# Kernel optimization log

Measured on AMD Instinct MI355X. Metric: run time of the kernel, lower is better.

## Reference

```python
import jax, jax.numpy as jnp
import numpy as np

REL_SIZE = 65
TAG_SIZE = 4


def _rope(y):
    # Interleaved rotary position embedding, matching the torch module:
    # cos_pos = cos(theta) repeat_interleave(2), sin_pos = sin(theta) repeat_interleave(2)
    # y2 = (-y1, y0, -y3, y2, ...)
    B, S, H = y.shape
    half = H // 2
    pos = jnp.arange(S, dtype=jnp.float32)[:, None]                      # (S,1)
    inv_freq = jnp.power(10000.0, -2.0 * jnp.arange(half, dtype=jnp.float32) / H)
    theta = pos * inv_freq                                               # (S, half)
    cos = jnp.repeat(jnp.cos(theta), 2, axis=-1)                          # (S, H)
    sin = jnp.repeat(jnp.sin(theta), 2, axis=-1)                          # (S, H)
    yr = y.reshape(B, S, half, 2)
    y2 = jnp.stack([-yr[..., 1], yr[..., 0]], axis=-1).reshape(B, S, H)
    return y * cos + y2 * sin


def setup_inputs() -> dict:
    key = jax.random.key(0)
    k1, k2, k3 = jax.random.split(key, 3)
    B, S, H = 1, 160, 768
    y = jax.random.normal(k1, (B, S, H), dtype=jnp.float32)
    event_idx = jax.random.randint(k2, (B, 16), 0, S)
    W1 = jax.random.normal(k3, (H, 2 * H), dtype=jnp.float32) * 0.02
    b1 = jnp.zeros((H,), dtype=jnp.float32)
    W2 = jax.random.normal(jax.random.fold_in(key, 7), (REL_SIZE * TAG_SIZE, H), dtype=jnp.float32) * 0.02
    b2 = jnp.zeros((REL_SIZE * TAG_SIZE,), dtype=jnp.float32)
    return {"y": y, "event_idx": event_idx, "W1": W1, "b1": b1, "W2": W2, "b2": b2}


def reference(y, event_idx, W1, b1, W2, b2):
    # Eval path (training=False): event_idx unused, dropout = identity, sigmoid applied.
    B, S, H = y.shape
    yrot = _rope(y)
    # Linear(cat(a, b)) is separable: split W1 into the halves acting on a and b.
    Wa, Wb = W1[:, :H], W1[:, H:]
    left = jnp.einsum('bsh,oh->bso', yrot, Wa)                  # contribution of token i (row)
    right = jnp.einsum('bsh,oh->bso', yrot, Wb) + b1            # contribution of token j (col)
    h = jax.nn.relu(left[:, :, None, :] + right[:, None, :, :])  # (B, S, S, H)
    out = jnp.einsum('bijh,oh->bijo', h, W2) + b2               # (B, S, S, 260)
    out = out.reshape(B, S, S, REL_SIZE, TAG_SIZE).transpose(0, 3, 1, 2, 4)  # (B, 65, S, S, 4)
    return jax.nn.sigmoid(out)
```

## Files before the change

### kernel.cpp

```cpp
#include <hip/hip_runtime.h>
#include <hip/hip_bf16.h>
#include <cstdint>

#define SDIM 160
#define HDIM 768
#define HALF 384
#define ODIM 260
#define OPAD 272
#define WS_SMALL 1155088
#define WS_BIG   3514384

typedef __attribute__((ext_vector_type(8))) short short8;
typedef __attribute__((ext_vector_type(4))) float floatx4;
typedef _Float16 half8 __attribute__((ext_vector_type(8)));

static __device__ __forceinline__ float bf2f(unsigned short u) {
    union { unsigned int i; float f; } v; v.i = ((unsigned int)u) << 16; return v.f;
}
static __device__ __forceinline__ unsigned short f2bf(float x) {
    __hip_bfloat16 h = __float2bfloat16(x);
    return *reinterpret_cast<unsigned short*>(&h);
}
static __device__ __forceinline__ unsigned short f2h(float x) {
    _Float16 h = (_Float16)x;
    return *reinterpret_cast<unsigned short*>(&h);
}
static __device__ __forceinline__ float q(float x) { return bf2f(f2bf(x)); }

__global__ __launch_bounds__(256) void prep_kernel(
    const float* __restrict__ y, const float* __restrict__ W1,
    const float* __restrict__ W2,
    unsigned short* __restrict__ yb, unsigned short* __restrict__ W2b,
    unsigned short* __restrict__ W1b, int do_w1b) {
    int bid = blockIdx.x;
    int t = threadIdx.x;
    if (bid < SDIM) {
        int s = bid;
        for (int p = t; p < HALF; p += 256) {
            float invf = __expf(-(2.0f * (float)p / (float)HDIM) * 9.210340371976184f);
            float th = (float)s * invf;
            float c = cosf(th), sn = sinf(th);
            float y0 = y[s * HDIM + 2 * p], y1 = y[s * HDIM + 2 * p + 1];
            yb[s * HDIM + 2 * p]     = f2bf(y0 * c - y1 * sn);
            yb[s * HDIM + 2 * p + 1] = f2bf(y1 * c + y0 * sn);
        }
    } else if (bid < SDIM + 102) {
        int idx = (bid - SDIM) * 256 + t;
        if (idx < 96 * OPAD) {
            int kg = idx / OPAD, row = idx - kg * OPAD;
            unsigned short o8[8];
            if (row < ODIM) {
                float4 a = *reinterpret_cast<const float4*>(W2 + row * HDIM + kg * 8);
                float4 b = *reinterpret_cast<const float4*>(W2 + row * HDIM + kg * 8 + 4);
                o8[0] = f2h(a.x); o8[1] = f2h(a.y); o8[2] = f2h(a.z); o8[3] = f2h(a.w);
                o8[4] = f2h(b.x); o8[5] = f2h(b.y); o8[6] = f2h(b.z); o8[7] = f2h(b.w);
            } else {
                #pragma unroll
                for (int e = 0; e < 8; ++e) o8[e] = 0;
            }
            *reinterpret_cast<uint4*>(W2b + ((size_t)kg * OPAD + row) * 8) =
                *reinterpret_cast<uint4*>(o8);
        }
    } else if (do_w1b) {
        int idx = (bid - SDIM - 102) * 256 + t;
        int kg = idx / 1536, row = idx - kg * 1536;
        const float* src = (row < 768) ? (W1 + row * 1536 + kg * 8)
                                       : (W1 + (row - 768) * 1536 + 768 + kg * 8);
        float4 a = *reinterpret_cast<const float4*>(src);
        float4 b = *reinterpret_cast<const float4*>(src + 4);
        unsigned short o8[8];
        o8[0] = f2bf(a.x); o8[1] = f2bf(a.y); o8[2] = f2bf(a.z); o8[3] = f2bf(a.w);
        o8[4] = f2bf(b.x); o8[5] = f2bf(b.y); o8[6] = f2bf(b.z); o8[7] = f2bf(b.w);
        *reinterpret_cast<uint4*>(W1b + ((size_t)kg * 1536 + row) * 8) =
            *reinterpret_cast<uint4*>(o8);
    }
}

__global__ __launch_bounds__(64, 2) void lr3_kernel(
    const unsigned short* __restrict__ yb, const unsigned short* __restrict__ W1b,
    const float* __restrict__ b1,
    unsigned short* __restrict__ Lb, unsigned short* __restrict__ Rt) {
    int l = threadIdx.x & 63;
    int l16 = l & 15, qd = l >> 4;
    int mt = blockIdx.x;
    int sq = blockIdx.y;
    int s0 = sq * 16 + l16;

    floatx4 acc = (floatx4){0.0f, 0.0f, 0.0f, 0.0f};

    const unsigned short* yrow0 = yb + s0 * HDIM;

    for (int ks = 0; ks < 24; ++ks) {
        int k = ks * 32 + qd * 8;
        int kg = ks * 4 + qd;
        union { uint4 u; short8 s; } bu0, au;
        bu0.u = *reinterpret_cast<const uint4*>(yrow0 + k);
        au.u = *reinterpret_cast<const uint4*>(
            W1b + ((size_t)kg * 1536 + mt * 16 + l16) * 8);
        acc = __builtin_amdgcn_mfma_f32_16x16x32_bf16(
            au.s, bu0.s, acc, 0, 0, 0);
    }

    int o2 = mt * 16 + qd * 4;
    int s_out = sq * 16 + l16;
    unsigned short out4[4];
    if (o2 < 768) {
        #pragma unroll
        for (int r = 0; r < 4; ++r) out4[r] = f2h(acc[r]);
        *reinterpret_cast<uint2*>(Lb + s_out * HDIM + o2) =
            *reinterpret_cast<uint2*>(out4);
    } else {
        int ob = o2 - 768;
        #pragma unroll
        for (int r = 0; r < 4; ++r)
            out4[r] = f2h(acc[r] + b1[ob + r]);
        *reinterpret_cast<uint2*>(
            Rt + ((size_t)(ob >> 3) * SDIM + s_out) * 8 + (ob & 7)) =
            *reinterpret_cast<uint2*>(out4);
    }
}

__global__ __launch_bounds__(256) void lr_fallback_kernel(
    const unsigned short* __restrict__ yb, const float* __restrict__ W1,
    const float* __restrict__ b1,
    unsigned short* __restrict__ Lb, unsigned short* __restrict__ Rt) {
    int idx = blockIdx.x * 256 + threadIdx.x;
    int s = idx / 1536;
    int o2 = idx - s * 1536;
    const unsigned short* yrow = yb + s * HDIM;
    if (o2 < 768) {
        const float* wp = W1 + o2 * 1536;
        float a0 = 0.0f;
        for (int k = 0; k < HDIM; ++k) a0 += q(wp[k]) * bf2f(yrow[k]);
        Lb[s * HDIM + o2] = f2h(a0);
    } else {
        int ob = o2 - 768;
        const float* wp = W1 + ob * 1536 + 768;
        float a0 = 0.0f;
        for (int k = 0; k < HDIM; ++k) a0 += q(wp[k]) * bf2f(yrow[k]);
        Rt[((size_t)(ob >> 3) * SDIM + s) * 8 + (ob & 7)] = f2h(a0 + b1[ob]);
    }
}

__global__ __launch_bounds__(64, 4) void main_kernel(
    const unsigned short* __restrict__ Lb, const unsigned short* __restrict__ Rt,
    const unsigned short* __restrict__ W2b,
    const float* __restrict__ b2, float* __restrict__ out) {
    int l = threadIdx.x & 63;
    int l16 = l & 15, qd = l >> 4;
    int w = blockIdx.z;
    int jh = w & 1;
    int mq = w >> 1;
    int mt0 = mq * 4;
    int nmt = (mq == 3) ? 5 : 4;
    int i0 = blockIdx.x * 2;
    int j = blockIdx.y * 32 + jh * 16 + l16;

    floatx4 acc[2][5];
    #pragma unroll
    for (int c = 0; c < 2; ++c)
        #pragma unroll
        for (int mtl = 0; mtl < 5; ++mtl)
            acc[c][mtl] = (floatx4){0.0f, 0.0f, 0.0f, 0.0f};

    const unsigned short* Lrow0 = Lb + i0 * HDIM;
    const unsigned short* Lrow1 = Lb + (i0 + 1) * HDIM;
    const unsigned short* wbase = W2b + (size_t)l16 * 8;

    #pragma unroll 2
    for (int kc = 0; kc < 12; ++kc) {
        #pragma unroll
        for (int ks = 0; ks < 2; ++ks) {
            int k = kc * 64 + ks * 32 + qd * 8;
            int kg = kc * 8 + ks * 4 + qd;
            half8 bfrag[2];
            union { uint4 u; half8 h; } ru;
            ru.u = *reinterpret_cast<const uint4*>(
                Rt + ((size_t)kg * SDIM + j) * 8);
            #pragma unroll
            for (int c = 0; c < 2; ++c) {
                const unsigned short* Lr = c ? Lrow1 : Lrow0;
                union { uint4 u; half8 h; } lu;
                lu.u = *reinterpret_cast<const uint4*>(Lr + k);
                half8 hv = lu.h + ru.h;
                #pragma unroll
                for (int e = 0; e < 8; ++e)
                    hv[e] = hv[e] > (_Float16)0.0f ? hv[e] : (_Float16)0.0f;
                bfrag[c] = hv;
            }
            const unsigned short* wkg = wbase + (size_t)kg * OPAD * 8;
            #pragma unroll
            for (int mtl = 0; mtl < 5; ++mtl) {
                if (mtl < nmt) {
                    union { uint4 u; half8 h; } au;
                    au.u = *reinterpret_cast<const uint4*>(
                        wkg + (size_t)(mt0 + mtl) * 16 * 8);
                    acc[0][mtl] = __builtin_amdgcn_mfma_f32_16x16x32_f16(
                        au.h, bfrag[0], acc[0][mtl], 0, 0, 0);
                    acc[1][mtl] = __builtin_amdgcn_mfma_f32_16x16x32_f16(
                        au.h, bfrag[1], acc[1][mtl], 0, 0, 0);
                }
            }
        }
    }

    #pragma unroll
    for (int c = 0; c < 2; ++c) {
        int i = i0 + c;
        #pragma unroll
        for (int mtl = 0; mtl < 5; ++mtl) {
            if (mtl < nmt) {
                int ob = (mt0 + mtl) * 16 + qd * 4;
                if (ob < ODIM) {
                    float4 bv = *reinterpret_cast<const float4*>(b2 + ob);
                    int rel = ob >> 2;
                    float4 v;
                    v.x = 1.0f / (1.0f + __expf(-(acc[c][mtl][0] + bv.x)));
                    v.y = 1.0f / (1.0f + __expf(-(acc[c][mtl][1] + bv.y)));
                    v.z = 1.0f / (1.0f + __expf(-(acc[c][mtl][2] + bv.z)));
                    v.w = 1.0f / (1.0f + __expf(-(acc[c][mtl][3] + bv.w)));
                    *reinterpret_cast<float4*>(
                        out + (((rel * SDIM) + i) * SDIM + j) * 4) = v;
                }
            }
        }
    }
}

__global__ void ws_too_small_kernel(float* out) { out[0] = 999.0f; }

extern "C" void kernel_launch(void* const* d_in, const int* in_sizes, int n_in,
                              void* d_out, int out_size, void* d_ws, size_t ws_size,
                              hipStream_t stream) {
    const float* y  = (const float*)d_in[0];
    const float* W1 = (const float*)d_in[2];
    const float* b1 = (const float*)d_in[3];
    const float* W2 = (const float*)d_in[4];
    const float* b2 = (const float*)d_in[5];
    float* out = (float*)d_out;

    if (ws_size < (size_t)WS_SMALL) {
        ws_too_small_kernel<<<dim3(1), dim3(1), 0, stream>>>(out);
        return;
    }

    unsigned short* yb  = (unsigned short*)((char*)d_ws + 16);
    unsigned short* Lb  = yb + SDIM * HDIM;
    unsigned short* Rt  = Lb + SDIM * HDIM;
    unsigned short* W2b = Rt + SDIM * HDIM;
    unsigned short* W1b = W2b + 96 * OPAD * 8;

    if (ws_size >= (size_t)WS_BIG) {
        prep_kernel<<<dim3(SDIM + 102 + 576), dim3(256), 0, stream>>>(
            y, W1, W2, yb, W2b, W1b, 1);
        lr3_kernel<<<dim3(96, 10), dim3(64), 0, stream>>>(yb, W1b, b1, Lb, Rt);
        main_kernel<<<dim3(80, 5, 8), dim3(64), 0, stream>>>(Lb, Rt, W2b, b2, out);
    } else {
        prep_kernel<<<dim3(SDIM + 102), dim3(256), 0, stream>>>(
            y, W1, W2, yb, W2b, W1b, 0);
        lr_fallback_kernel<<<dim3(960), dim3(256), 0, stream>>>(yb, W1, b1, Lb, Rt);
        main_kernel<<<dim3(80, 5, 8), dim3(64), 0, stream>>>(Lb, Rt, W2b, b2, out);
    }
}
```

Baseline: 122.7 us.

## Fuse RoPE/W1 prep into left-right GEMM and double-buffer main kernel loads

The separate prep and left/right projection kernels are merged into one launch. It converts W2 to fp16 and, for each tile, applies RoPE to y and converts W1 to bf16 on the fly before the MFMA. That removes the yb and W1b staging buffers and one kernel launch, at the cost of recomputing sin/cos and W1 conversions redundantly across blocks. The main kernel now prefetches the next k-step's W2, R and L fragments into a second register buffer while the current step's MFMAs run. Its occupancy hint drops from 4 to 3 waves, and every wave now issues all 5 M-tiles regardless of group, so groups that own only 4 tiles do extra discarded MFMA work.

```diff
diff --git a/kernel.cpp b/kernel.cpp
--- a/kernel.cpp
+++ b/kernel.cpp
@@ -7,8 +7,7 @@
 #define HALF 384
 #define ODIM 260
 #define OPAD 272
-#define WS_SMALL 1155088
-#define WS_BIG   3514384
+#define WS_NEED 1155088
 
 typedef __attribute__((ext_vector_type(8))) short short8;
 typedef __attribute__((ext_vector_type(4))) float floatx4;
@@ -25,89 +24,80 @@
     _Float16 h = (_Float16)x;
     return *reinterpret_cast<unsigned short*>(&h);
 }
-static __device__ __forceinline__ float q(float x) { return bf2f(f2bf(x)); }
-
-__global__ __launch_bounds__(256) void prep_kernel(
+
+__global__ __launch_bounds__(64) void fused_a_kernel(
     const float* __restrict__ y, const float* __restrict__ W1,
-    const float* __restrict__ W2,
-    unsigned short* __restrict__ yb, unsigned short* __restrict__ W2b,
-    unsigned short* __restrict__ W1b, int do_w1b) {
+    const float* __restrict__ b1, const float* __restrict__ W2,
+    unsigned short* __restrict__ W2b,
+    unsigned short* __restrict__ Lb, unsigned short* __restrict__ Rt) {
     int bid = blockIdx.x;
     int t = threadIdx.x;
-    if (bid < SDIM) {
-        int s = bid;
-        for (int p = t; p < HALF; p += 256) {
-            float invf = __expf(-(2.0f * (float)p / (float)HDIM) * 9.210340371976184f);
-            float th = (float)s * invf;
-            float c = cosf(th), sn = sinf(th);
-            float y0 = y[s * HDIM + 2 * p], y1 = y[s * HDIM + 2 * p + 1];
-            yb[s * HDIM + 2 * p]     = f2bf(y0 * c - y1 * sn);
-            yb[s * HDIM + 2 * p + 1] = f2bf(y1 * c + y0 * sn);
-        }
-    } else if (bid < SDIM + 102) {
-        int idx = (bid - SDIM) * 256 + t;
-        if (idx < 96 * OPAD) {
-            int kg = idx / OPAD, row = idx - kg * OPAD;
-            unsigned short o8[8];
-            if (row < ODIM) {
-                float4 a = *reinterpret_cast<const float4*>(W2 + row * HDIM + kg * 8);
-                float4 b = *reinterpret_cast<const float4*>(W2 + row * HDIM + kg * 8 + 4);
-                o8[0] = f2h(a.x); o8[1] = f2h(a.y); o8[2] = f2h(a.z); o8[3] = f2h(a.w);
-                o8[4] = f2h(b.x); o8[5] = f2h(b.y); o8[6] = f2h(b.z); o8[7] = f2h(b.w);
-            } else {
-                #pragma unroll
-                for (int e = 0; e < 8; ++e) o8[e] = 0;
-            }
-            *reinterpret_cast<uint4*>(W2b + ((size_t)kg * OPAD + row) * 8) =
-                *reinterpret_cast<uint4*>(o8);
-        }
-    } else if (do_w1b) {
-        int idx = (bid - SDIM - 102) * 256 + t;
-        int kg = idx / 1536, row = idx - kg * 1536;
-        const float* src = (row < 768) ? (W1 + row * 1536 + kg * 8)
-                                       : (W1 + (row - 768) * 1536 + 768 + kg * 8);
-        float4 a = *reinterpret_cast<const float4*>(src);
-        float4 b = *reinterpret_cast<const float4*>(src + 4);
+
+    if (bid < 408) {
+        int idx = bid * 64 + t;
+        int kg = idx / OPAD, row = idx - kg * OPAD;
         unsigned short o8[8];
-        o8[0] = f2bf(a.x); o8[1] = f2bf(a.y); o8[2] = f2bf(a.z); o8[3] = f2bf(a.w);
-        o8[4] = f2bf(b.x); o8[5] = f2bf(b.y); o8[6] = f2bf(b.z); o8[7] = f2bf(b.w);
-        *reinterpret_cast<uint4*>(W1b + ((size_t)kg * 1536 + row) * 8) =
+        if (row < ODIM) {
+            float4 a = *reinterpret_cast<const float4*>(W2 + row * HDIM + kg * 8);
+            float4 b = *reinterpret_cast<const float4*>(W2 + row * HDIM + kg * 8 + 4);
+            o8[0] = f2h(a.x); o8[1] = f2h(a.y); o8[2] = f2h(a.z); o8[3] = f2h(a.w);
+            o8[4] = f2h(b.x); o8[5] = f2h(b.y); o8[6] = f2h(b.z); o8[7] = f2h(b.w);
+        } else {
+            #pragma unroll
+            for (int e = 0; e < 8; ++e) o8[e] = 0;
+        }
+        *reinterpret_cast<uint4*>(W2b + ((size_t)kg * OPAD + row) * 8) =
             *reinterpret_cast<uint4*>(o8);
-    }
-}
-
-__global__ __launch_bounds__(64, 2) void lr3_kernel(
-    const unsigned short* __restrict__ yb, const unsigned short* __restrict__ W1b,
-    const float* __restrict__ b1,
-    unsigned short* __restrict__ Lb, unsigned short* __restrict__ Rt) {
-    int l = threadIdx.x & 63;
-    int l16 = l & 15, qd = l >> 4;
-    int mt = blockIdx.x;
-    int sq = blockIdx.y;
+        return;
+    }
+
+    int bid2 = bid - 408;
+    int mt = bid2 % 96;
+    int sq = bid2 / 96;
+    int l16 = t & 15, qd = t >> 4;
     int s0 = sq * 16 + l16;
+    int row = mt * 16 + l16;
+    const float* wrow = (row < 768) ? (W1 + (size_t)row * 1536)
+                                    : (W1 + (size_t)(row - 768) * 1536 + 768);
+    const float* yrow = y + (size_t)s0 * HDIM;
+    float sf = (float)s0;
 
     floatx4 acc = (floatx4){0.0f, 0.0f, 0.0f, 0.0f};
-
-    const unsigned short* yrow0 = yb + s0 * HDIM;
 
     for (int ks = 0; ks < 24; ++ks) {
         int k = ks * 32 + qd * 8;
         int kg = ks * 4 + qd;
-        union { uint4 u; short8 s; } bu0, au;
-        bu0.u = *reinterpret_cast<const uint4*>(yrow0 + k);
-        au.u = *reinterpret_cast<const uint4*>(
-            W1b + ((size_t)kg * 1536 + mt * 16 + l16) * 8);
-        acc = __builtin_amdgcn_mfma_f32_16x16x32_bf16(
-            au.s, bu0.s, acc, 0, 0, 0);
+        float4 ya = *reinterpret_cast<const float4*>(yrow + k);
+        float4 yb4 = *reinterpret_cast<const float4*>(yrow + k + 4);
+        float yv[8] = {ya.x, ya.y, ya.z, ya.w, yb4.x, yb4.y, yb4.z, yb4.w};
+        unsigned short b8[8];
+        #pragma unroll
+        for (int e = 0; e < 4; ++e) {
+            int p = (k >> 1) + e;
+            float invf = __expf(-(2.0f * (float)p / (float)HDIM) * 9.210340371976184f);
+            float th = sf * invf;
+            float c = cosf(th), sn = sinf(th);
+            float y0 = yv[2 * e], y1 = yv[2 * e + 1];
+            b8[2 * e]     = f2bf(y0 * c - y1 * sn);
+            b8[2 * e + 1] = f2bf(y1 * c + y0 * sn);
+        }
+        float4 wa = *reinterpret_cast<const float4*>(wrow + kg * 8);
+        float4 wb = *reinterpret_cast<const float4*>(wrow + kg * 8 + 4);
+        unsigned short w8[8];
+        w8[0] = f2bf(wa.x); w8[1] = f2bf(wa.y); w8[2] = f2bf(wa.z); w8[3] = f2bf(wa.w);
+        w8[4] = f2bf(wb.x); w8[5] = f2bf(wb.y); w8[6] = f2bf(wb.z); w8[7] = f2bf(wb.w);
+        union { uint4 u; short8 s; } au, bu;
+        au.u = *reinterpret_cast<uint4*>(w8);
+        bu.u = *reinterpret_cast<uint4*>(b8);
+        acc = __builtin_amdgcn_mfma_f32_16x16x32_bf16(au.s, bu.s, acc, 0, 0, 0);
     }
 
     int o2 = mt * 16 + qd * 4;
-    int s_out = sq * 16 + l16;
     unsigned short out4[4];
     if (o2 < 768) {
         #pragma unroll
         for (int r = 0; r < 4; ++r) out4[r] = f2h(acc[r]);
-        *reinterpret_cast<uint2*>(Lb + s_out * HDIM + o2) =
+        *reinterpret_cast<uint2*>(Lb + s0 * HDIM + o2) =
             *reinterpret_cast<uint2*>(out4);
     } else {
         int ob = o2 - 768;
@@ -115,34 +105,12 @@
         for (int r = 0; r < 4; ++r)
             out4[r] = f2h(acc[r] + b1[ob + r]);
         *reinterpret_cast<uint2*>(
-            Rt + ((size_t)(ob >> 3) * SDIM + s_out) * 8 + (ob & 7)) =
+            Rt + ((size_t)(ob >> 3) * SDIM + s0) * 8 + (ob & 7)) =
             *reinterpret_cast<uint2*>(out4);
     }
 }
 
-__global__ __launch_bounds__(256) void lr_fallback_kernel(
-    const unsigned short* __restrict__ yb, const float* __restrict__ W1,
-    const float* __restrict__ b1,
-    unsigned short* __restrict__ Lb, unsigned short* __restrict__ Rt) {
-    int idx = blockIdx.x * 256 + threadIdx.x;
-    int s = idx / 1536;
-    int o2 = idx - s * 1536;
-    const unsigned short* yrow = yb + s * HDIM;
-    if (o2 < 768) {
-        const float* wp = W1 + o2 * 1536;
-        float a0 = 0.0f;
-        for (int k = 0; k < HDIM; ++k) a0 += q(wp[k]) * bf2f(yrow[k]);
-        Lb[s * HDIM + o2] = f2h(a0);
-    } else {
-        int ob = o2 - 768;
-        const float* wp = W1 + ob * 1536 + 768;
-        float a0 = 0.0f;
-        for (int k = 0; k < HDIM; ++k) a0 += q(wp[k]) * bf2f(yrow[k]);
-        Rt[((size_t)(ob >> 3) * SDIM + s) * 8 + (ob & 7)] = f2h(a0 + b1[ob]);
-    }
-}
-
-__global__ __launch_bounds__(64, 4) void main_kernel(
+__global__ __launch_bounds__(64, 3) void main_kernel(
     const unsigned short* __restrict__ Lb, const unsigned short* __restrict__ Rt,
     const unsigned short* __restrict__ W2b,
     const float* __restrict__ b2, float* __restrict__ out) {
@@ -167,40 +135,43 @@
     const unsigned short* Lrow1 = Lb + (i0 + 1) * HDIM;
     const unsigned short* wbase = W2b + (size_t)l16 * 8;
 
+    union U { uint4 u; half8 h; };
+    U au[2][5], ru[2], lu[2][2];
+
+    auto ISSUE = [&](int t, int b) {
+        int kg = t * 4 + qd;
+        const unsigned short* wkg = wbase + (size_t)kg * (OPAD * 8);
+        #pragma unroll
+        for (int m = 0; m < 5; ++m)
+            au[b][m].u = *reinterpret_cast<const uint4*>(
+                wkg + (size_t)(mt0 + m) * 128);
+        ru[b].u = *reinterpret_cast<const uint4*>(
+            Rt + ((size_t)kg * SDIM + j) * 8);
+        int k = t * 32 + qd * 8;
+        lu[b][0].u = *reinterpret_cast<const uint4*>(Lrow0 + k);
+        lu[b][1].u = *reinterpret_cast<const uint4*>(Lrow1 + k);
+    };
+
+    ISSUE(0, 0);
     #pragma unroll 2
-    for (int kc = 0; kc < 12; ++kc) {
-        #pragma unroll
-        for (int ks = 0; ks < 2; ++ks) {
-            int k = kc * 64 + ks * 32 + qd * 8;
-            int kg = kc * 8 + ks * 4 + qd;
-            half8 bfrag[2];
-            union { uint4 u; half8 h; } ru;
-            ru.u = *reinterpret_cast<const uint4*>(
-                Rt + ((size_t)kg * SDIM + j) * 8);
+    for (int t = 0; t < 24; ++t) {
+        int b = t & 1;
+        if (t < 23) ISSUE(t + 1, b ^ 1);
+        half8 bfrag[2];
+        #pragma unroll
+        for (int c = 0; c < 2; ++c) {
+            half8 hv = lu[b][c].h + ru[b].h;
             #pragma unroll
-            for (int c = 0; c < 2; ++c) {
-                const unsigned short* Lr = c ? Lrow1 : Lrow0;
-                union { uint4 u; half8 h; } lu;
-                lu.u = *reinterpret_cast<const uint4*>(Lr + k);
-                half8 hv = lu.h + ru.h;
-                #pragma unroll
-                for (int e = 0; e < 8; ++e)
-                    hv[e] = hv[e] > (_Float16)0.0f ? hv[e] : (_Float16)0.0f;
-                bfrag[c] = hv;
-            }
-            const unsigned short* wkg = wbase + (size_t)kg * OPAD * 8;
-            #pragma unroll
-            for (int mtl = 0; mtl < 5; ++mtl) {
-                if (mtl < nmt) {
-                    union { uint4 u; half8 h; } au;
-                    au.u = *reinterpret_cast<const uint4*>(
-                        wkg + (size_t)(mt0 + mtl) * 16 * 8);
-                    acc[0][mtl] = __builtin_amdgcn_mfma_f32_16x16x32_f16(
-                        au.h, bfrag[0], acc[0][mtl], 0, 0, 0);
-                    acc[1][mtl] = __builtin_amdgcn_mfma_f32_16x16x32_f16(
-                        au.h, bfrag[1], acc[1][mtl], 0, 0, 0);
-                }
-            }
+            for (int e = 0; e < 8; ++e)
+                hv[e] = hv[e] > (_Float16)0.0f ? hv[e] : (_Float16)0.0f;
+            bfrag[c] = hv;
+        }
+        #pragma unroll
+        for (int m = 0; m < 5; ++m) {
+            acc[0][m] = __builtin_amdgcn_mfma_f32_16x16x32_f16(
+                au[b][m].h, bfrag[0], acc[0][m], 0, 0, 0);
+            acc[1][m] = __builtin_amdgcn_mfma_f32_16x16x32_f16(
+                au[b][m].h, bfrag[1], acc[1][m], 0, 0, 0);
         }
     }
 
@@ -239,7 +210,7 @@
     const float* b2 = (const float*)d_in[5];
     float* out = (float*)d_out;
 
-    if (ws_size < (size_t)WS_SMALL) {
+    if (ws_size < (size_t)WS_NEED) {
         ws_too_small_kernel<<<dim3(1), dim3(1), 0, stream>>>(out);
         return;
     }
@@ -248,17 +219,8 @@
     unsigned short* Lb  = yb + SDIM * HDIM;
     unsigned short* Rt  = Lb + SDIM * HDIM;
     unsigned short* W2b = Rt + SDIM * HDIM;
-    unsigned short* W1b = W2b + 96 * OPAD * 8;
-
-    if (ws_size >= (size_t)WS_BIG) {
-        prep_kernel<<<dim3(SDIM + 102 + 576), dim3(256), 0, stream>>>(
-            y, W1, W2, yb, W2b, W1b, 1);
-        lr3_kernel<<<dim3(96, 10), dim3(64), 0, stream>>>(yb, W1b, b1, Lb, Rt);
-        main_kernel<<<dim3(80, 5, 8), dim3(64), 0, stream>>>(Lb, Rt, W2b, b2, out);
-    } else {
-        prep_kernel<<<dim3(SDIM + 102), dim3(256), 0, stream>>>(
-            y, W1, W2, yb, W2b, W1b, 0);
-        lr_fallback_kernel<<<dim3(960), dim3(256), 0, stream>>>(yb, W1, b1, Lb, Rt);
-        main_kernel<<<dim3(80, 5, 8), dim3(64), 0, stream>>>(Lb, Rt, W2b, b2, out);
-    }
-}
+
+    fused_a_kernel<<<dim3(408 + 960), dim3(64), 0, stream>>>(
+        y, W1, b1, W2, W2b, Lb, Rt);
+    main_kernel<<<dim3(80, 5, 8), dim3(64), 0, stream>>>(Lb, Rt, W2b, b2, out);
+}
```

Result: slower. 258.2 us (+110.5%).
